# Kernel tuning notes

Measured on AMD Instinct MI355X. Metric: run time of the kernel, lower is better.

Reference implementation:

```python
import jax, jax.numpy as jnp
import numpy as np

D_MODEL = 768
N_HEADS = 12
HEAD_DIM = D_MODEL // N_HEADS
FFN_DIM = 3072
MAX_WAVELENGTH = 10000.0
ROPE_PERCENT = 0.5
NORM_EPS = 1e-5


def setup_inputs() -> dict:
    key = jax.random.key(0)
    ks = jax.random.split(key, 12)
    B, C, S = 2, 16, 128
    init = lambda k, shape: (jax.random.normal(k, shape, dtype=jnp.float32) * 0.02)
    return {
        "hidden_state": jax.random.normal(ks[0], (B, C, S, D_MODEL), dtype=jnp.float32),
        "wq": init(ks[1], (D_MODEL, D_MODEL)), "bq": jnp.zeros((D_MODEL,), jnp.float32),
        "wk": init(ks[2], (D_MODEL, D_MODEL)), "bk": jnp.zeros((D_MODEL,), jnp.float32),
        "wv": init(ks[3], (D_MODEL, D_MODEL)), "bv": jnp.zeros((D_MODEL,), jnp.float32),
        "wo": init(ks[4], (D_MODEL, D_MODEL)), "bo": jnp.zeros((D_MODEL,), jnp.float32),
        "attn_biases": init(ks[5], (N_HEADS, 2)),
        "ln1_g": jnp.ones((D_MODEL,), jnp.float32), "ln1_b": jnp.zeros((D_MODEL,), jnp.float32),
        "ln3_g": jnp.ones((D_MODEL,), jnp.float32), "ln3_b": jnp.zeros((D_MODEL,), jnp.float32),
        "w1": init(ks[6], (D_MODEL, FFN_DIM)), "b1": jnp.zeros((FFN_DIM,), jnp.float32),
        "w2": init(ks[7], (FFN_DIM, D_MODEL)), "b2": jnp.zeros((D_MODEL,), jnp.float32),
    }


def _layernorm(x, g, b):
    mu = jnp.mean(x, axis=-1, keepdims=True)
    var = jnp.mean(jnp.square(x - mu), axis=-1, keepdims=True)
    return (x - mu) * jax.lax.rsqrt(var + NORM_EPS) * g + b


def _apply_p_rope(x, positions):
    # x: [B, H, T, head_dim]; p-RoPE: only rope_percent of frequency bands rotate.
    half = HEAD_DIM // 2
    rope_angles = int(ROPE_PERCENT * HEAD_DIM) // 2  # 16
    fraction = 2.0 * jnp.arange(rope_angles, dtype=jnp.float32) / HEAD_DIM
    timescale = jnp.concatenate([
        MAX_WAVELENGTH ** fraction,
        jnp.full((half - rope_angles,), jnp.inf, dtype=jnp.float32),
    ])  # [half]
    angles = positions[:, None].astype(jnp.float32) / timescale[None, :]  # [T, half]
    sin = jnp.sin(angles)[None, None]  # [1,1,T,half]
    cos = jnp.cos(angles)[None, None]
    x1, x2 = jnp.split(x, 2, axis=-1)
    return jnp.concatenate([x1 * cos - x2 * sin, x2 * cos + x1 * sin], axis=-1)


def _forward(hidden_state, wq, bq, wk, bk, wv, bv, wo, bo, attn_biases,
             ln1_g, ln1_b, ln3_g, ln3_b, w1, b1, w2, b2):
    B, C, S, D = hidden_state.shape
    T = C * S
    flat = hidden_state.reshape(B, T, D)

    # --- attention sublayer (pre-norm) ---
    ni = _layernorm(flat, ln1_g, ln1_b)
    scaling = HEAD_DIM ** -0.5
    q = (ni @ wq + bq) * scaling
    k = ni @ wk + bk
    v = ni @ wv + bv
    to_heads = lambda t: t.reshape(B, T, N_HEADS, HEAD_DIM).transpose(0, 2, 1, 3)
    q, k, v = to_heads(q), to_heads(k), to_heads(v)  # [B,H,T,hd]

    positions = jnp.arange(T)
    k = _apply_p_rope(k, positions)
    q = _apply_p_rope(q, positions)

    scores = jnp.einsum("bhtd,bhsd->bhts", q, k)  # [B,H,T,T]
    variate_ids = positions // S
    same = (variate_ids[:, None] == variate_ids[None, :]).astype(scores.dtype)  # [T,T]
    variate_bias = (same[None, :, :] * attn_biases[:, 0][:, None, None]
                    + (1.0 - same[None, :, :]) * attn_biases[:, 1][:, None, None])  # [H,T,T]
    scores = scores + variate_bias[None]
    probs = jax.nn.softmax(scores, axis=-1)
    attn = jnp.einsum("bhts,bhsd->bhtd", probs, v)
    attn = attn.transpose(0, 2, 1, 3).reshape(B, T, D)
    attn = attn @ wo + bo

    flat = flat + attn  # residual (pre-norm -> no post-norm here)

    # --- feed-forward sublayer (pre-norm) ---
    ff_in = _layernorm(flat, ln3_g, ln3_b)
    ff = jax.nn.gelu(ff_in @ w1 + b1, approximate=False) @ w2 + b2
    flat = flat + ff

    return flat.reshape(B, C, S, D)


def reference(hidden_state, wq, bq, wk, bk, wv, bv, wo, bo, attn_biases,
              ln1_g, ln1_b, ln3_g, ln3_b, w1, b1, w2, b2):
    return _forward(hidden_state, wq, bq, wk, bk, wv, bv, wo, bo, attn_biases,
                    ln1_g, ln1_b, ln3_g, ln3_b, w1, b1, w2, b2)
```

## Files before the change

### kernel.cpp

```cpp
#include <hip/hip_runtime.h>
#include <cmath>


typedef __bf16 bf16_t;
typedef bf16_t bf16x8 __attribute__((ext_vector_type(8)));
typedef float floatx4 __attribute__((ext_vector_type(4)));

#define MFMA(a, b, c) __builtin_amdgcn_mfma_f32_16x16x32_bf16((a), (b), (c), 0, 0, 0)
#define LOG2E 1.44269504088896340736f

__device__ __forceinline__ bf16_t f2bf(float f) { return (bf16_t)f; }

__device__ __forceinline__ void g2l16(const void* g, void* l) {
  __builtin_amdgcn_global_load_lds(
      (const __attribute__((address_space(1))) unsigned int*)g,
      (__attribute__((address_space(3))) unsigned int*)l, 16, 0, 0);
}

__device__ __forceinline__ void lds_fence() {
  asm volatile("s_waitcnt lgkmcnt(0)" ::: "memory");
}
__device__ __forceinline__ void wait_vm4() {
  asm volatile("s_waitcnt vmcnt(4)" ::: "memory");
}

struct PrepP {
  const float *wq, *wk, *wv, *wo, *w1, *w2;
  bf16_t *wqkvT, *woT, *w1T, *w2T;
  const float *hs, *g1, *be1;
  bf16_t* ni;
};

__global__ __launch_bounds__(256) void k_prep(PrepP p) {
  __shared__ float shm[32 * 33];
  const int bid = blockIdx.x;
  if (bid < 6912) {
    const float* in;
    bf16_t* out;
    int R, C, tx, ty;
    if (bid < 2304) {
      int m = bid / 576, lo = bid % 576;
      in = (m == 0) ? p.wq : (m == 1) ? p.wk : (m == 2) ? p.wv : p.wo;
      out = (m < 3) ? p.wqkvT + (size_t)m * 768 * 768 : p.woT;
      R = 768; C = 768; tx = lo % 24; ty = lo / 24;
    } else if (bid < 4608) {
      int lo = bid - 2304;
      in = p.w1; out = p.w1T; R = 768; C = 3072; tx = lo % 96; ty = lo / 96;
    } else {
      int lo = bid - 4608;
      in = p.w2; out = p.w2T; R = 3072; C = 768; tx = lo % 24; ty = lo / 24;
    }
    const int c0 = tx * 32, r0 = ty * 32;
    const int lx = threadIdx.x & 31, ly = threadIdx.x >> 5;
#pragma unroll
    for (int p4 = 0; p4 < 4; p4++) {
      int r = ly + p4 * 8;
      shm[r * 33 + lx] = in[(size_t)(r0 + r) * C + c0 + lx];
    }
    __syncthreads();
#pragma unroll
    for (int p4 = 0; p4 < 4; p4++) {
      int r = ly + p4 * 8;
      out[(size_t)(c0 + r) * R + r0 + lx] = f2bf(shm[lx * 33 + r]);
    }
  } else {
    const int row = bid - 6912;
    const float* xr = p.hs + (size_t)row * 768;
    const int t = threadIdx.x;
    float v0 = xr[t], v1 = xr[t + 256], v2 = xr[t + 512];
    float s = v0 + v1 + v2;
    float s2 = v0 * v0 + v1 * v1 + v2 * v2;
#pragma unroll
    for (int off = 32; off; off >>= 1) {
      s += __shfl_xor(s, off);
      s2 += __shfl_xor(s2, off);
    }
    const int w = t >> 6;
    if ((t & 63) == 0) { shm[w] = s; shm[4 + w] = s2; }
    __syncthreads();
    s = shm[0] + shm[1] + shm[2] + shm[3];
    s2 = shm[4] + shm[5] + shm[6] + shm[7];
    const float mu = s * (1.0f / 768.0f);
    const float var = s2 * (1.0f / 768.0f) - mu * mu;
    const float rstd = rsqrtf(var + 1e-5f);
    bf16_t* orow = p.ni + (size_t)row * 768;
    orow[t]       = f2bf((v0 - mu) * rstd * p.g1[t]       + p.be1[t]);
    orow[t + 256] = f2bf((v1 - mu) * rstd * p.g1[t + 256] + p.be1[t + 256]);
    orow[t + 512] = f2bf((v2 - mu) * rstd * p.g1[t + 512] + p.be1[t + 512]);
  }
}

__global__ __launch_bounds__(256) void k_layernorm(
    const float* __restrict__ x, const float* __restrict__ g,
    const float* __restrict__ b, bf16_t* __restrict__ out) {
  const int row = blockIdx.x;
  const float* xr = x + (size_t)row * 768;
  const int t = threadIdx.x;
  float v0 = xr[t], v1 = xr[t + 256], v2 = xr[t + 512];
  float s = v0 + v1 + v2;
  float s2 = v0 * v0 + v1 * v1 + v2 * v2;
#pragma unroll
  for (int off = 32; off; off >>= 1) {
    s += __shfl_xor(s, off);
    s2 += __shfl_xor(s2, off);
  }
  __shared__ float ra[4], rb[4];
  const int w = t >> 6;
  if ((t & 63) == 0) { ra[w] = s; rb[w] = s2; }
  __syncthreads();
  s = ra[0] + ra[1] + ra[2] + ra[3];
  s2 = rb[0] + rb[1] + rb[2] + rb[3];
  const float mu = s * (1.0f / 768.0f);
  const float var = s2 * (1.0f / 768.0f) - mu * mu;
  const float rstd = rsqrtf(var + 1e-5f);
  bf16_t* orow = out + (size_t)row * 768;
  orow[t]       = f2bf((v0 - mu) * rstd * g[t]       + b[t]);
  orow[t + 256] = f2bf((v1 - mu) * rstd * g[t + 256] + b[t + 256]);
  orow[t + 512] = f2bf((v2 - mu) * rstd * g[t + 512] + b[t + 512]);
}

struct GemmP {
  const bf16_t* A;
  const bf16_t* Bt;
  int M, N, K, mode;
  const float* bias0;
  const float* bias1;
  const float* bias2;
  float* outF;
  bf16_t* outB0;
  bf16_t* outB1;
  bf16_t* outB2;
};

__global__ __launch_bounds__(256, 3) void k_gemm(GemmP p) {
  __shared__ bf16_t lds[18432];
  const int tid = threadIdx.x;
  const int lane = tid & 63, wave = tid >> 6;
  const int quad = lane >> 4, l15 = lane & 15;
  const int wm = (wave >> 1) * 64, wn = (wave & 1) * 64;
  const int m0 = blockIdx.y * 128, n0 = blockIdx.x * 128;

  const char* gA[4];
  const char* gB[4];
#pragma unroll
  for (int pp = 0; pp < 4; pp++) {
    int slot = wave * 256 + pp * 64 + lane;
    int r = slot >> 3;
    int c8 = ((slot & 7) ^ (r & 7)) << 3;
    gA[pp] = (const char*)(p.A + (size_t)(m0 + r) * p.K + c8);
    gB[pp] = (const char*)(p.Bt + (size_t)(n0 + r) * p.K + c8);
  }

  int offA[4], offB[4];
#pragma unroll
  for (int i = 0; i < 4; i++) {
    int ra = wm + i * 16 + l15;
    offA[i] = ra * 64 + ((quad * 8) ^ ((ra & 7) << 3));
    int rb = wn + i * 16 + l15;
    offB[i] = rb * 64 + ((quad * 8) ^ ((rb & 7) << 3));
  }

  const floatx4 z4 = {0.f, 0.f, 0.f, 0.f};
  floatx4 acc[4][4];
#pragma unroll
  for (int i = 0; i < 4; i++)
#pragma unroll
    for (int j = 0; j < 4; j++) acc[i][j] = z4;

  const int KT = p.K >> 6;
  bf16_t* Ad = lds + wave * 2048;
  bf16_t* Bd = lds + 8192 + wave * 2048;

  for (int kt = 0; kt < KT; kt++) {
    const size_t kb = (size_t)kt * 128;
#pragma unroll
    for (int pp = 0; pp < 4; pp++) {
      g2l16(gA[pp] + kb, Ad + pp * 512);
      g2l16(gB[pp] + kb, Bd + pp * 512);
    }
    __syncthreads();
#pragma unroll
    for (int ks = 0; ks < 2; ks++) {
      bf16x8 af[4], bfr[4];
#pragma unroll
      for (int i = 0; i < 4; i++) {
        af[i] = *(const bf16x8*)(lds + (offA[i] ^ (ks * 32)));
        bfr[i] = *(const bf16x8*)(lds + 8192 + (offB[i] ^ (ks * 32)));
      }
#pragma unroll
      for (int i = 0; i < 4; i++)
#pragma unroll
        for (int j = 0; j < 4; j++) acc[i][j] = MFMA(af[i], bfr[j], acc[i][j]);
    }
    __syncthreads();
  }

  char* scr = (char*)lds + wave * 9216;

  if (p.mode == 0) {
    const int gnw = n0 + wn;
    const int region = gnw / 768;
    const int rem = gnw - region * 768;
    const int h = rem >> 6;
    const int b = (m0 + wm) >> 11;
    const int t0 = (m0 + wm) & 2047;
    const float* bias = (region == 0) ? p.bias0 : (region == 1 ? p.bias1 : p.bias2);
    float bb[4];
#pragma unroll
    for (int j = 0; j < 4; j++) bb[j] = bias[h * 64 + j * 16 + l15];
    bf16_t* sb = (bf16_t*)scr;
    if (region < 2) {
      const float scale = (region == 0) ? 0.125f * LOG2E : 1.0f;
      const float inv_ts = exp2f(-(float)l15 * (13.287712379549449f / 32.0f));
#pragma unroll
      for (int i = 0; i < 4; i++) {
#pragma unroll
        for (int reg = 0; reg < 4; reg++) {
          int tl = i * 16 + quad * 4 + reg;
          float sn, cs;
          __sincosf((float)(t0 + tl) * inv_ts, &sn, &cs);
          float v0 = (acc[i][0][reg] + bb[0]) * scale;
          float v1 = (acc[i][1][reg] + bb[1]) * scale;
          float v2 = (acc[i][2][reg] + bb[2]) * scale;
          float v3 = (acc[i][3][reg] + bb[3]) * scale;
          sb[tl * 72 + l15]      = f2bf(v0 * cs - v2 * sn);
          sb[tl * 72 + 16 + l15] = f2bf(v1);
          sb[tl * 72 + 32 + l15] = f2bf(v2 * cs + v0 * sn);
          sb[tl * 72 + 48 + l15] = f2bf(v3);
        }
      }
      __syncthreads();
      bf16_t* outp = (region == 0) ? p.outB0 : p.outB1;
      bf16_t* ob = outp + (((size_t)(b * 12 + h) * 2048 + t0) << 6);
#pragma unroll
      for (int pp = 0; pp < 8; pp++) {
        int row = pp * 8 + (lane >> 3), ch = (lane & 7) << 3;
        *(bf16x8*)(ob + row * 64 + ch) = *(const bf16x8*)&sb[row * 72 + ch];
      }
    } else {
#pragma unroll
      for (int i = 0; i < 4; i++)
#pragma unroll
        for (int j = 0; j < 4; j++)
#pragma unroll
          for (int reg = 0; reg < 4; reg++)
            sb[(j * 16 + l15) * 72 + i * 16 + quad * 4 + reg] =
                f2bf(acc[i][j][reg] + bb[j]);
      __syncthreads();
      bf16_t* ob = p.outB2 + (((size_t)(b * 12 + h)) << 17) + t0;
#pragma unroll
      for (int pp = 0; pp < 8; pp++) {
        int d = pp * 8 + (lane >> 3), ch = (lane & 7) << 3;
        *(bf16x8*)(ob + (size_t)d * 2048 + ch) = *(const bf16x8*)&sb[d * 72 + ch];
      }
    }
  } else {
    bf16_t* sb = (bf16_t*)scr;
    float bb[4];
#pragma unroll
    for (int j = 0; j < 4; j++) bb[j] = p.bias0[n0 + wn + j * 16 + l15];
#pragma unroll
    for (int i = 0; i < 4; i++)
#pragma unroll
      for (int j = 0; j < 4; j++)
#pragma unroll
        for (int reg = 0; reg < 4; reg++) {
          int tl = i * 16 + quad * 4 + reg;
          float x = acc[i][j][reg] + bb[j];
          float gv = 0.5f * x * (1.0f + erff(x * 0.70710678118654752f));
          sb[tl * 72 + j * 16 + l15] = f2bf(gv);
        }
    __syncthreads();
#pragma unroll
    for (int pp = 0; pp < 8; pp++) {
      int row = pp * 8 + (lane >> 3), ch = (lane & 7) << 3;
      *(bf16x8*)(p.outB0 + (size_t)(m0 + wm + row) * p.N + n0 + wn + ch) =
          *(const bf16x8*)&sb[row * 72 + ch];
    }
  }
}

__global__ __launch_bounds__(256, 4) void k_gemm64(
    const bf16_t* __restrict__ A, const bf16_t* __restrict__ Bt, int N, int K,
    const float* __restrict__ bias, const float* __restrict__ resid,
    float* __restrict__ outF) {
  __shared__ bf16_t lds[16384];
  const int tid = threadIdx.x;
  const int lane = tid & 63, wave = tid >> 6;
  const int quad = lane >> 4, l15 = lane & 15;
  const int wm = (wave >> 1) * 32, wn = (wave & 1) * 32;
  const int m0 = blockIdx.y * 64, n0 = blockIdx.x * 64;

  const char* gA[4];
  const char* gB[4];
#pragma unroll
  for (int pp = 0; pp < 4; pp++) {
    int slot = wave * 256 + pp * 64 + lane;
    int r = slot >> 4;
    int c = ((slot & 15) ^ (r & 7)) << 3;
    gA[pp] = (const char*)(A + (size_t)(m0 + r) * K + c);
    gB[pp] = (const char*)(Bt + (size_t)(n0 + r) * K + c);
  }

  const floatx4 z4 = {0.f, 0.f, 0.f, 0.f};
  floatx4 acc[2][2];
#pragma unroll
  for (int i = 0; i < 2; i++)
#pragma unroll
    for (int j = 0; j < 2; j++) acc[i][j] = z4;

  const int KT = K >> 7;
  bf16_t* Ad = lds + wave * 2048;
  bf16_t* Bd = lds + 8192 + wave * 2048;

  for (int kt = 0; kt < KT; kt++) {
    const size_t kb = (size_t)kt * 256;
#pragma unroll
    for (int pp = 0; pp < 4; pp++) {
      g2l16(gA[pp] + kb, Ad + pp * 512);
      g2l16(gB[pp] + kb, Bd + pp * 512);
    }
    __syncthreads();
#pragma unroll
    for (int ks = 0; ks < 4; ks++) {
      bf16x8 af[2], bfr[2];
#pragma unroll
      for (int i = 0; i < 2; i++) {
        int ra = wm + i * 16 + l15;
        af[i] = *(const bf16x8*)(lds + ra * 128 +
                                 (((ks * 4 + quad) ^ (ra & 7)) << 3));
        int rb = wn + i * 16 + l15;
        bfr[i] = *(const bf16x8*)(lds + 8192 + rb * 128 +
                                  (((ks * 4 + quad) ^ (rb & 7)) << 3));
      }
#pragma unroll
      for (int i = 0; i < 2; i++)
#pragma unroll
        for (int j = 0; j < 2; j++) acc[i][j] = MFMA(af[i], bfr[j], acc[i][j]);
    }
    __syncthreads();
  }

  float* s4 = (float*)lds + wave * 1024;
#pragma unroll
  for (int i = 0; i < 2; i++)
#pragma unroll
    for (int j = 0; j < 2; j++)
#pragma unroll
      for (int reg = 0; reg < 4; reg++)
        s4[(i * 16 + quad * 4 + reg) * 32 + j * 16 + l15] = acc[i][j][reg];
  __syncthreads();
#pragma unroll
  for (int pp = 0; pp < 4; pp++) {
    int row = pp * 8 + (lane >> 3);
    int c4 = (lane & 7) * 4;
    floatx4 v = *(const floatx4*)&s4[row * 32 + c4];
    size_t goff = (size_t)(m0 + wm + row) * N + n0 + wn + c4;
    floatx4 rv = *(const floatx4*)(resid + goff);
    floatx4 bv = *(const floatx4*)(bias + n0 + wn + c4);
    *(floatx4*)(outF + goff) = v + rv + bv;
  }
}

__global__ __launch_bounds__(256, 2) void k_flash(
    const bf16_t* __restrict__ qh, const bf16_t* __restrict__ kh,
    const bf16_t* __restrict__ vt, const float* __restrict__ ab,
    bf16_t* __restrict__ attnA) {
  __shared__ bf16_t sm[35328];

  const int tid = threadIdx.x, lane = tid & 63, wave = tid >> 6;
  const int quad = lane >> 4, l15 = lane & 15;
  const int qtile = blockIdx.x, bh = blockIdx.y;
  const int h = bh % 12, bq = bh / 12;
  const int myv = qtile >> 1;

  bf16_t* wb = sm + wave * 8704;
  bf16_t* Kb0 = wb;
  bf16_t* Vs = wb + 2048;
  bf16_t* Pb = wb + 6144;

  const bf16_t* Qg = qh + ((size_t)bh * 2048 + qtile * 64) * 64;
  const bf16_t* Kg = kh + ((size_t)bh * 2048 + wave * 16) * 64;

  const char* gK[2];
#pragma unroll
  for (int i = 0; i < 2; i++) {
    int sl = i * 8 + (lane >> 3);
    int cs = (lane & 7) ^ (sl & 7);
    gK[i] = (const char*)(Kg + sl * 64 + cs * 8);
  }
  const char* gV[2];
#pragma unroll
  for (int i = 0; i < 2; i++) {
    int d = i * 32 + (lane >> 1);
    int hs = (lane & 1) ^ ((d >> 2) & 1);
    gV[i] = (const char*)(vt + ((size_t)(bh * 64 + d)) * 2048 + wave * 16 + hs * 8);
  }

  bf16x8 qf[4][2];
#pragma unroll
  for (int mt = 0; mt < 4; mt++)
#pragma unroll
    for (int ks = 0; ks < 2; ks++)
      qf[mt][ks] = *(const bf16x8*)(Qg + (size_t)(mt * 16 + l15) * 64 +
                                    ks * 32 + quad * 8);

  int offKr[2];
#pragma unroll
  for (int ks = 0; ks < 2; ks++)
    offKr[ks] = l15 * 64 + ((((ks << 2) + quad) ^ (l15 & 7)) << 3);
  int offV[4];
#pragma unroll
  for (int nt = 0; nt < 4; nt++) {
    int d = nt * 16 + l15;
    offV[nt] = (quad >> 1) * 1024 + d * 16 +
               (((quad & 1) ^ ((d >> 2) & 1)) << 3);
  }

  const floatx4 z4 = {0.f, 0.f, 0.f, 0.f};
  floatx4 oacc[4][4];
  float l_lane[4][4];
#pragma unroll
  for (int mt = 0; mt < 4; mt++)
#pragma unroll
    for (int nt = 0; nt < 4; nt++) oacc[mt][nt] = z4;
#pragma unroll
  for (int mt = 0; mt < 4; mt++)
#pragma unroll
    for (int r = 0; r < 4; r++) l_lane[mt][r] = 0.f;

  const float bc_same = ab[h * 2] * LOG2E;
  const float bc_diff = ab[h * 2 + 1] * LOG2E;

  g2l16(gK[0], Kb0);
  g2l16(gK[1], Kb0 + 512);
  g2l16(gV[0], Vs);
  g2l16(gV[1], Vs + 512);

  for (int kv = 0; kv < 32; kv++) {
    const int nkv = (kv + 1) & 31;
    {
      const size_t kbK = (size_t)nkv * 8192, kbV = (size_t)nkv * 128;
      bf16_t* Kd = Kb0 + (nkv & 1) * 1024;
      bf16_t* Vd = Vs + ((((nkv >> 1) & 1) << 1) + (nkv & 1)) * 1024;
      g2l16(gK[0] + kbK, Kd);
      g2l16(gK[1] + kbK, Kd + 512);
      g2l16(gV[0] + kbV, Vd);
      g2l16(gV[1] + kbV, Vd + 512);
    }
    wait_vm4();

    const bf16_t* Kc = Kb0 + (kv & 1) * 1024;
    floatx4 sacc[4] = {z4, z4, z4, z4};
#pragma unroll
    for (int ks = 0; ks < 2; ks++) {
      const bf16x8 kf = *(const bf16x8*)(Kc + offKr[ks]);
#pragma unroll
      for (int mt = 0; mt < 4; mt++)
        sacc[mt] = MFMA(qf[mt][ks], kf, sacc[mt]);
    }

    const float bc = ((kv >> 1) == myv) ? bc_same : bc_diff;
    const int pw = (kv & 1) * 16 + l15;
#pragma unroll
    for (int mt = 0; mt < 4; mt++)
#pragma unroll
      for (int reg = 0; reg < 4; reg++) {
        float pv = exp2f(sacc[mt][reg] + bc);
        l_lane[mt][reg] += pv;
        Pb[(mt * 16 + quad * 4 + reg) * 40 + pw] = f2bf(pv);
      }

    if (kv & 1) {
      lds_fence();
      bf16x8 pf[4];
#pragma unroll
      for (int mt = 0; mt < 4; mt++)
        pf[mt] = *(const bf16x8*)(Pb + (mt * 16 + l15) * 40 + quad * 8);
      const int vb = ((kv >> 1) & 1) * 2048;
#pragma unroll
      for (int nt = 0; nt < 4; nt++) {
        const bf16x8 vf = *(const bf16x8*)(Vs + vb + offV[nt]);
#pragma unroll
        for (int mt = 0; mt < 4; mt++)
          oacc[mt][nt] = MFMA(pf[mt], vf, oacc[mt][nt]);
      }
    }
  }

#pragma unroll
  for (int mt = 0; mt < 4; mt++)
#pragma unroll
    for (int reg = 0; reg < 4; reg++) {
      float v = l_lane[mt][reg];
      v += __shfl_xor(v, 1);
      v += __shfl_xor(v, 2);
      v += __shfl_xor(v, 4);
      v += __shfl_xor(v, 8);
      l_lane[mt][reg] = v;
    }
  float* lred = (float*)(sm + 34816);
  if (l15 == 0) {
#pragma unroll
    for (int mt = 0; mt < 4; mt++)
#pragma unroll
      for (int reg = 0; reg < 4; reg++)
        lred[wave * 64 + mt * 16 + quad * 4 + reg] = l_lane[mt][reg];
  }
#pragma unroll
  for (int mt = 0; mt < 4; mt++)
#pragma unroll
    for (int nt = 0; nt < 4; nt++)
#pragma unroll
      for (int reg = 0; reg < 4; reg++)
        wb[(mt * 16 + quad * 4 + reg) * 64 + nt * 16 + l15] =
            f2bf(oacc[mt][nt][reg]);
  __syncthreads();

  const int q = tid >> 2, dg = (tid & 3) * 16;
  const float inv =
      1.0f / (lred[q] + lred[64 + q] + lred[128 + q] + lred[192 + q]);
  float o[16];
#pragma unroll
  for (int j = 0; j < 16; j++) o[j] = 0.f;
#pragma unroll
  for (int w = 0; w < 4; w++) {
    const bf16x8 a = *(const bf16x8*)(sm + w * 8704 + q * 64 + dg);
    const bf16x8 b = *(const bf16x8*)(sm + w * 8704 + q * 64 + dg + 8);
#pragma unroll
    for (int j = 0; j < 8; j++) {
      o[j] += (float)a[j];
      o[8 + j] += (float)b[j];
    }
  }
  bf16x8 r0, r1;
#pragma unroll
  for (int j = 0; j < 8; j++) {
    r0[j] = f2bf(o[j] * inv);
    r1[j] = f2bf(o[8 + j] * inv);
  }
  bf16_t* outp =
      attnA + ((size_t)(bq * 2048 + qtile * 64 + q)) * 768 + h * 64 + dg;
  *(bf16x8*)outp = r0;
  *(bf16x8*)(outp + 8) = r1;
}

extern "C" void kernel_launch(void* const* d_in, const int* in_sizes, int n_in,
                              void* d_out, int out_size, void* d_ws,
                              size_t ws_size, hipStream_t stream) {
  const float* hs  = (const float*)d_in[0];
  const float* wq  = (const float*)d_in[1];
  const float* bq  = (const float*)d_in[2];
  const float* wk  = (const float*)d_in[3];
  const float* bk  = (const float*)d_in[4];
  const float* wv  = (const float*)d_in[5];
  const float* bv  = (const float*)d_in[6];
  const float* wo  = (const float*)d_in[7];
  const float* bo  = (const float*)d_in[8];
  const float* ab  = (const float*)d_in[9];
  const float* g1  = (const float*)d_in[10];
  const float* be1 = (const float*)d_in[11];
  const float* g3  = (const float*)d_in[12];
  const float* be3 = (const float*)d_in[13];
  const float* w1  = (const float*)d_in[14];
  const float* b1  = (const float*)d_in[15];
  const float* w2  = (const float*)d_in[16];
  const float* b2  = (const float*)d_in[17];

  char* ws = (char*)d_ws;
  size_t off = 0;
  auto alloc = [&](size_t bytes) -> void* {
    void* p = ws + off;
    off += (bytes + 255) & ~(size_t)255;
    return p;
  };
  bf16_t* wqkvT = (bf16_t*)alloc((size_t)2304 * 768 * 2);
  bf16_t* woT   = (bf16_t*)alloc((size_t)768 * 768 * 2);
  bf16_t* w1T   = (bf16_t*)alloc((size_t)3072 * 768 * 2);
  bf16_t* w2T   = (bf16_t*)alloc((size_t)768 * 3072 * 2);
  bf16_t* ni    = (bf16_t*)alloc((size_t)4096 * 768 * 2);
  bf16_t* qhB   = (bf16_t*)alloc((size_t)24 * 2048 * 64 * 2);
  bf16_t* khB   = (bf16_t*)alloc((size_t)24 * 2048 * 64 * 2);
  bf16_t* vtB   = (bf16_t*)alloc((size_t)24 * 64 * 2048 * 2);
  bf16_t* attnA = (bf16_t*)alloc((size_t)4096 * 768 * 2);
  float*  resid1 = (float*)alloc((size_t)4096 * 768 * 4);
  bf16_t* ffn1o = qhB;

  PrepP pp = {wq, wk, wv, wo, w1, w2, wqkvT, woT, w1T, w2T, hs, g1, be1, ni};
  k_prep<<<11008, 256, 0, stream>>>(pp);

  GemmP gqkv = {ni, wqkvT, 4096, 2304, 768, 0,
                bq, bk, bv, nullptr, qhB, khB, vtB};
  k_gemm<<<dim3(18, 32), 256, 0, stream>>>(gqkv);

  k_flash<<<dim3(32, 24), 256, 0, stream>>>(qhB, khB, vtB, ab, attnA);

  k_gemm64<<<dim3(12, 64), 256, 0, stream>>>(attnA, woT, 768, 768, bo, hs,
                                             resid1);

  k_layernorm<<<4096, 256, 0, stream>>>(resid1, g3, be3, ni);

  GemmP gf1 = {ni, w1T, 4096, 3072, 768, 2,
               b1, nullptr, nullptr, nullptr, ffn1o, nullptr, nullptr};
  k_gemm<<<dim3(24, 32), 256, 0, stream>>>(gf1);

  k_gemm64<<<dim3(12, 64), 256, 0, stream>>>(ffn1o, w2T, 768, 3072, b2,
                                             resid1, (float*)d_out);
}
```

Measured before the change: 287.8 us.

## Keep attention probabilities in registers via permlane swaps instead of LDS

The flash-attention kernel now computes S transposed (K as the A operand) so each lane holds probabilities for one query row. It packs them to bf16 with v_cvt_pk_bf16 and rearranges them with permlane32/16 swaps into the PV operand layout, removing the LDS round trip and the lgkmcnt fence for P. The bias is folded into the accumulator init, and the row sums reduce across quads. The freed LDS lets occupancy rise to 3 blocks per CU, at the cost of more register pressure and an untested, layout-sensitive permute sequence.

```diff
diff --git a/kernel.cpp b/kernel.cpp
--- a/kernel.cpp
+++ b/kernel.cpp
@@ -5,6 +5,7 @@
 typedef __bf16 bf16_t;
 typedef bf16_t bf16x8 __attribute__((ext_vector_type(8)));
 typedef float floatx4 __attribute__((ext_vector_type(4)));
+typedef unsigned int u32x4 __attribute__((ext_vector_type(4)));
 
 #define MFMA(a, b, c) __builtin_amdgcn_mfma_f32_16x16x32_bf16((a), (b), (c), 0, 0, 0)
 #define LOG2E 1.44269504088896340736f
@@ -17,11 +18,23 @@
       (__attribute__((address_space(3))) unsigned int*)l, 16, 0, 0);
 }
 
-__device__ __forceinline__ void lds_fence() {
-  asm volatile("s_waitcnt lgkmcnt(0)" ::: "memory");
-}
 __device__ __forceinline__ void wait_vm4() {
   asm volatile("s_waitcnt vmcnt(4)" ::: "memory");
+}
+__device__ __forceinline__ void wait_vm0() {
+  asm volatile("s_waitcnt vmcnt(0)" ::: "memory");
+}
+
+__device__ __forceinline__ unsigned cvt_pk_bf16(float lo, float hi) {
+  unsigned r;
+  asm("v_cvt_pk_bf16_f32 %0, %1, %2" : "=v"(r) : "v"(lo), "v"(hi));
+  return r;
+}
+__device__ __forceinline__ void pl32swap(unsigned& a, unsigned& b) {
+  asm("v_permlane32_swap_b32 %0, %1" : "+v"(a), "+v"(b));
+}
+__device__ __forceinline__ void pl16swap(unsigned& a, unsigned& b) {
+  asm("v_permlane16_swap_b32 %0, %1" : "+v"(a), "+v"(b));
 }
 
 struct PrepP {
@@ -362,11 +375,11 @@
   }
 }
 
-__global__ __launch_bounds__(256, 2) void k_flash(
+__global__ __launch_bounds__(256, 3) void k_flash(
     const bf16_t* __restrict__ qh, const bf16_t* __restrict__ kh,
     const bf16_t* __restrict__ vt, const float* __restrict__ ab,
     bf16_t* __restrict__ attnA) {
-  __shared__ bf16_t sm[35328];
+  __shared__ bf16_t sm[25088];
 
   const int tid = threadIdx.x, lane = tid & 63, wave = tid >> 6;
   const int quad = lane >> 4, l15 = lane & 15;
@@ -374,10 +387,9 @@
   const int h = bh % 12, bq = bh / 12;
   const int myv = qtile >> 1;
 
-  bf16_t* wb = sm + wave * 8704;
+  bf16_t* wb = sm + wave * 6144;
   bf16_t* Kb0 = wb;
   bf16_t* Vs = wb + 2048;
-  bf16_t* Pb = wb + 6144;
 
   const bf16_t* Qg = qh + ((size_t)bh * 2048 + qtile * 64) * 64;
   const bf16_t* Kg = kh + ((size_t)bh * 2048 + wave * 16) * 64;
@@ -419,15 +431,14 @@
 
   const floatx4 z4 = {0.f, 0.f, 0.f, 0.f};
   floatx4 oacc[4][4];
-  float l_lane[4][4];
+  float l_mt[4];
+  unsigned pA[4], pB[4];
 #pragma unroll
   for (int mt = 0; mt < 4; mt++)
 #pragma unroll
     for (int nt = 0; nt < 4; nt++) oacc[mt][nt] = z4;
 #pragma unroll
-  for (int mt = 0; mt < 4; mt++)
-#pragma unroll
-    for (int r = 0; r < 4; r++) l_lane[mt][r] = 0.f;
+  for (int mt = 0; mt < 4; mt++) l_mt[mt] = 0.f;
 
   const float bc_same = ab[h * 2] * LOG2E;
   const float bc_diff = ab[h * 2 + 1] * LOG2E;
@@ -437,6 +448,7 @@
   g2l16(gV[0], Vs);
   g2l16(gV[1], Vs + 512);
 
+#pragma unroll 2
   for (int kv = 0; kv < 32; kv++) {
     const int nkv = (kv + 1) & 31;
     {
@@ -451,61 +463,69 @@
     wait_vm4();
 
     const bf16_t* Kc = Kb0 + (kv & 1) * 1024;
-    floatx4 sacc[4] = {z4, z4, z4, z4};
+    const float bc = ((kv >> 1) == myv) ? bc_same : bc_diff;
+    floatx4 sacc[4];
+#pragma unroll
+    for (int mt = 0; mt < 4; mt++) sacc[mt] = (floatx4){bc, bc, bc, bc};
 #pragma unroll
     for (int ks = 0; ks < 2; ks++) {
       const bf16x8 kf = *(const bf16x8*)(Kc + offKr[ks]);
 #pragma unroll
       for (int mt = 0; mt < 4; mt++)
-        sacc[mt] = MFMA(qf[mt][ks], kf, sacc[mt]);
-    }
-
-    const float bc = ((kv >> 1) == myv) ? bc_same : bc_diff;
-    const int pw = (kv & 1) * 16 + l15;
+        sacc[mt] = MFMA(kf, qf[mt][ks], sacc[mt]);
+    }
+
+    if (!(kv & 1)) {
+#pragma unroll
+      for (int mt = 0; mt < 4; mt++) {
+        float p0 = exp2f(sacc[mt][0]), p1 = exp2f(sacc[mt][1]);
+        float p2 = exp2f(sacc[mt][2]), p3 = exp2f(sacc[mt][3]);
+        l_mt[mt] += (p0 + p1) + (p2 + p3);
+        pA[mt] = cvt_pk_bf16(p0, p1);
+        pB[mt] = cvt_pk_bf16(p2, p3);
+      }
+    } else {
+      bf16x8 vf[4];
+      const int vb = ((kv >> 1) & 1) * 2048;
+#pragma unroll
+      for (int nt = 0; nt < 4; nt++)
+        vf[nt] = *(const bf16x8*)(Vs + vb + offV[nt]);
+#pragma unroll
+      for (int mt = 0; mt < 4; mt++) {
+        float p0 = exp2f(sacc[mt][0]), p1 = exp2f(sacc[mt][1]);
+        float p2 = exp2f(sacc[mt][2]), p3 = exp2f(sacc[mt][3]);
+        l_mt[mt] += (p0 + p1) + (p2 + p3);
+        unsigned b0 = cvt_pk_bf16(p0, p1);
+        unsigned b1 = cvt_pk_bf16(p2, p3);
+        unsigned a0 = pA[mt], a1 = pB[mt];
+        pl32swap(a0, b0);
+        pl16swap(a0, b0);
+        pl32swap(a1, b1);
+        pl16swap(a1, b1);
+        u32x4 w;
+        w[0] = a0; w[1] = a1; w[2] = b0; w[3] = b1;
+        const bf16x8 pf = __builtin_bit_cast(bf16x8, w);
+#pragma unroll
+        for (int nt = 0; nt < 4; nt++)
+          oacc[mt][nt] = MFMA(pf, vf[nt], oacc[mt][nt]);
+      }
+    }
+  }
+
+  wait_vm0();
+
+#pragma unroll
+  for (int mt = 0; mt < 4; mt++) {
+    float v = l_mt[mt];
+    v += __shfl_xor(v, 16);
+    v += __shfl_xor(v, 32);
+    l_mt[mt] = v;
+  }
+  float* lred = (float*)(sm + 24576);
+  if (quad == 0) {
 #pragma unroll
     for (int mt = 0; mt < 4; mt++)
-#pragma unroll
-      for (int reg = 0; reg < 4; reg++) {
-        float pv = exp2f(sacc[mt][reg] + bc);
-        l_lane[mt][reg] += pv;
-        Pb[(mt * 16 + quad * 4 + reg) * 40 + pw] = f2bf(pv);
-      }
-
-    if (kv & 1) {
-      lds_fence();
-      bf16x8 pf[4];
-#pragma unroll
-      for (int mt = 0; mt < 4; mt++)
-        pf[mt] = *(const bf16x8*)(Pb + (mt * 16 + l15) * 40 + quad * 8);
-      const int vb = ((kv >> 1) & 1) * 2048;
-#pragma unroll
-      for (int nt = 0; nt < 4; nt++) {
-        const bf16x8 vf = *(const bf16x8*)(Vs + vb + offV[nt]);
-#pragma unroll
-        for (int mt = 0; mt < 4; mt++)
-          oacc[mt][nt] = MFMA(pf[mt], vf, oacc[mt][nt]);
-      }
-    }
-  }
-
-#pragma unroll
-  for (int mt = 0; mt < 4; mt++)
-#pragma unroll
-    for (int reg = 0; reg < 4; reg++) {
-      float v = l_lane[mt][reg];
-      v += __shfl_xor(v, 1);
-      v += __shfl_xor(v, 2);
-      v += __shfl_xor(v, 4);
-      v += __shfl_xor(v, 8);
-      l_lane[mt][reg] = v;
-    }
-  float* lred = (float*)(sm + 34816);
-  if (l15 == 0) {
-#pragma unroll
-    for (int mt = 0; mt < 4; mt++)
-#pragma unroll
-      for (int reg = 0; reg < 4; reg++)
-        lred[wave * 64 + mt * 16 + quad * 4 + reg] = l_lane[mt][reg];
+      lred[wave * 64 + mt * 16 + l15] = l_mt[mt];
   }
 #pragma unroll
   for (int mt = 0; mt < 4; mt++)
@@ -525,8 +545,8 @@
   for (int j = 0; j < 16; j++) o[j] = 0.f;
 #pragma unroll
   for (int w = 0; w < 4; w++) {
-    const bf16x8 a = *(const bf16x8*)(sm + w * 8704 + q * 64 + dg);
-    const bf16x8 b = *(const bf16x8*)(sm + w * 8704 + q * 64 + dg + 8);
+    const bf16x8 a = *(const bf16x8*)(sm + w * 6144 + q * 64 + dg);
+    const bf16x8 b = *(const bf16x8*)(sm + w * 6144 + q * 64 + dg + 8);
 #pragma unroll
     for (int j = 0; j < 8; j++) {
       o[j] += (float)a[j];
```

Result: faster. 269.2 us (-6.5%).
